# Performance work log

Measured on AMD Instinct MI355X. Metric: run time of the kernel, lower is better.

Reference implementation:

```python
import jax, jax.numpy as jnp
import numpy as np

B, T, H, PRED = 16384, 8, 256, 12


def _cell(x, h, c, Wih, Whh, bih, bhh):
    # PyTorch LSTM gate order: i, f, g, o
    g = x @ Wih.T + h @ Whh.T + bih + bhh
    i, f, gg, o = jnp.split(g, 4, axis=-1)
    c = jax.nn.sigmoid(f) * c + jax.nn.sigmoid(i) * jnp.tanh(gg)
    h = jax.nn.sigmoid(o) * jnp.tanh(c)
    return h, c


def _run_seq(x, layers):
    # stacked LSTM over full sequence, zero initial state; x: [B, T, D]
    b = x.shape[0]
    inp = x
    hs, cs = [], []
    for (Wih, Whh, bih, bhh) in layers:
        h0 = jnp.zeros((b, Whh.shape[1]), x.dtype)

        def step(carry, xt, Wih=Wih, Whh=Whh, bih=bih, bhh=bhh):
            h, c = _cell(xt, carry[0], carry[1], Wih, Whh, bih, bhh)
            return (h, c), h

        (h, c), out = jax.lax.scan(step, (h0, h0), jnp.swapaxes(inp, 0, 1))
        inp = jnp.swapaxes(out, 0, 1)
        hs.append(h)
        cs.append(c)
    return inp, jnp.stack(hs), jnp.stack(cs)


def _step_stack(x, hs, cs, layers):
    # single-timestep pass through stacked LSTM; hs/cs: [L, B, H]
    inp = x
    nh, nc = [], []
    for l, (Wih, Whh, bih, bhh) in enumerate(layers):
        h, c = _cell(inp, hs[l], cs[l], Wih, Whh, bih, bhh)
        inp = h
        nh.append(h)
        nc.append(c)
    return inp, jnp.stack(nh), jnp.stack(nc)


def _forward(x, l1_Wih0, l1_Whh0, l1_bih0, l1_bhh0, l1_Wih1, l1_Whh1, l1_bih1, l1_bhh1,
             l2_Wih0, l2_Whh0, l2_bih0, l2_bhh0, l2_Wih1, l2_Whh1, l2_bih1, l2_bhh1,
             fc1_w, fc1_b, fc2_w, fc2_b):
    L1 = [(l1_Wih0, l1_Whh0, l1_bih0, l1_bhh0), (l1_Wih1, l1_Whh1, l1_bih1, l1_bhh1)]
    L2 = [(l2_Wih0, l2_Whh0, l2_bih0, l2_bhh0), (l2_Wih1, l2_Whh1, l2_bih1, l2_bhh1)]
    out1, h1, c1 = _run_seq(x, L1)           # encode observed track
    _, h2, c2 = _run_seq(out1, L2)
    pos = x[:, -1, :]

    def dec(carry, _):
        pos, h1, c1, h2, c2 = carry
        o1, h1, c1 = _step_stack(pos, h1, c1, L1)
        o2, h2, c2 = _step_stack(o1, h2, c2, L2)
        delta = jax.nn.relu(o2 @ fc1_w.T + fc1_b) @ fc2_w.T + fc2_b
        pos = pos + delta
        return (pos, h1, c1, h2, c2), pos

    _, preds = jax.lax.scan(dec, (pos, h1, c1, h2, c2), None, length=PRED)
    return jnp.swapaxes(preds, 0, 1)  # [B, PRED, 2]


def setup_inputs() -> dict:
    key = jax.random.key(0)
    ks = iter(jax.random.split(key, 32))
    s = 1.0 / np.sqrt(H)  # matches PyTorch LSTM/Linear init scale

    def mk(shape):
        return jax.random.uniform(next(ks), shape, jnp.float32, -s, s)

    d = {"x": jax.random.normal(next(ks), (B, T, 2), jnp.float32)}
    for name, in_dim in [("l1", 2), ("l2", H)]:
        for layer in range(2):
            di = in_dim if layer == 0 else H
            d[f"{name}_Wih{layer}"] = mk((4 * H, di))
            d[f"{name}_Whh{layer}"] = mk((4 * H, H))
            d[f"{name}_bih{layer}"] = mk((4 * H,))
            d[f"{name}_bhh{layer}"] = mk((4 * H,))
    d["fc1_w"] = mk((H, H))
    d["fc1_b"] = mk((H,))
    d["fc2_w"] = mk((2, H))
    d["fc2_b"] = mk((2,))
    return d


def reference(x, l1_Wih0, l1_Whh0, l1_bih0, l1_bhh0, l1_Wih1, l1_Whh1, l1_bih1, l1_bhh1,
              l2_Wih0, l2_Whh0, l2_bih0, l2_bhh0, l2_Wih1, l2_Whh1, l2_bih1, l2_bhh1,
              fc1_w, fc1_b, fc2_w, fc2_b):
    return _forward(x, l1_Wih0, l1_Whh0, l1_bih0, l1_bhh0, l1_Wih1, l1_Whh1, l1_bih1, l1_bhh1,
                    l2_Wih0, l2_Whh0, l2_bih0, l2_bhh0, l2_Wih1, l2_Whh1, l2_bih1, l2_bhh1,
                    fc1_w, fc1_b, fc2_w, fc2_b)
```

## Files before the change

### kernel.cpp

```cpp
#include <hip/hip_runtime.h>
#include <stdint.h>

#define Bsz   16384
#define Tseq  8
#define NPRED 12

typedef __attribute__((ext_vector_type(4))) float    f32x4;
typedef _Float16 h16;
typedef __attribute__((ext_vector_type(8))) _Float16 h16x8;

__device__ __forceinline__ float sigf(float x)   { return 1.f / (1.f + __expf(-x)); }
__device__ __forceinline__ float tanh_f(float x) { return 1.f - 2.f / (__expf(2.f * x) + 1.f); }

__device__ __forceinline__ void gload_lds16(const void* g, void* l) {
  __builtin_amdgcn_global_load_lds(
      (const __attribute__((address_space(1))) void*)g,
      (__attribute__((address_space(3))) void*)l, 16, 0, 0);
}

__global__ void mark_r11(float* __restrict__ out) {
  if (blockIdx.x == 0 && threadIdx.x < 64) out[threadIdx.x] = 1000.0f;
}
__global__ void seed_r11(float* __restrict__ pos, const float* __restrict__ x) {
  int b = blockIdx.x * 256 + threadIdx.x;
  pos[2 * b]     = x[(size_t)b * 16 + 14];
  pos[2 * b + 1] = x[(size_t)b * 16 + 15];
}

__global__ void pack_w(h16* __restrict__ dst, const float* __restrict__ W0,
                       const float* __restrict__ W1, int ksplit, int Kw, int Np,
                       int gatePack) {
  int idx = blockIdx.x * 256 + threadIdx.x;
  if (idx >= Np * Kw) return;
  int np = idx / Kw, k = idx - np * Kw;
  int n = np;
  if (gatePack) {
    int jb = np >> 7, wc = (np >> 6) & 1, gi = (np >> 4) & 3, jr = np & 15;
    n = gi * 256 + jb * 32 + wc * 16 + jr;
  }
  float w = (k < ksplit) ? W0[(size_t)n * ksplit + k]
                         : W1[(size_t)n * (Kw - ksplit) + (k - ksplit)];
  int KB = Kw >> 6;
  int jb = np >> 7, r = np & 127, kb = k >> 6;
  uint32_t byte = (uint32_t)(jb * KB + kb) * 16384u + (uint32_t)r * 128u
                + ((2u * (uint32_t)(k & 63)) ^ (uint32_t)((r & 7) << 4));
  *(h16*)((char*)dst + byte) = (h16)w;
}

__global__ void add_bias(float* __restrict__ dst, const float* __restrict__ a,
                         const float* __restrict__ b) {
  int i = blockIdx.x * 256 + threadIdx.x;
  if (i < 1024) dst[i] = a[i] + b[i];
}

__global__ void l0t0_pw(const float* __restrict__ x, const float* __restrict__ wih0,
                        const float* __restrict__ bias, float* __restrict__ Cst,
                        char* __restrict__ hout) {
  int gid = blockIdx.x * 256 + threadIdx.x;
  int b = gid >> 5, jb = (gid & 31) << 3;
  float x0 = x[(size_t)b * 16], x1 = x[(size_t)b * 16 + 1];
  float c[8]; h16 hh[8];
#pragma unroll
  for (int q = 0; q < 8; ++q) {
    int j = jb + q;
    float vi = bias[j]       + x0 * wih0[2 * j]           + x1 * wih0[2 * j + 1];
    float vg = bias[512 + j] + x0 * wih0[2 * (512 + j)]   + x1 * wih0[2 * (512 + j) + 1];
    float vo = bias[768 + j] + x0 * wih0[2 * (768 + j)]   + x1 * wih0[2 * (768 + j) + 1];
    float cn = sigf(vi) * tanh_f(vg);
    hh[q] = (h16)(sigf(vo) * tanh_f(cn));
    c[q] = cn;
  }
  *(f32x4*)(Cst + (size_t)b * 256 + jb)     = *(f32x4*)c;
  *(f32x4*)(Cst + (size_t)b * 256 + jb + 4) = *(f32x4*)(c + 4);
  *(h16x8*)(hout + (size_t)b * 512 + (((unsigned)jb * 2) ^ (unsigned)((b & 7) << 4))) = *(h16x8*)hh;
}

__device__ __forceinline__ void gemm_core(
    const char* A0, const char* A1, const char* Wp, int KB, int by, int m0,
    char* ldsA, char* ldsB, int tid, f32x4 acc[4][4]) {
  const int wave = tid >> 6, lane = tid & 63;
  const int rowa = tid >> 3;
  const int chb  = (tid & 7) * 16;

#pragma unroll
  for (int m = 0; m < 4; m++)
#pragma unroll
    for (int n = 0; n < 4; n++)
#pragma unroll
      for (int e = 0; e < 4; e++) acc[m][n][e] = 0.f;

  const char* aCur   = A0 + (size_t)(m0 + rowa) * 512 + chb;
  const char* a1Base = A1 + (size_t)(m0 + rowa) * 512 + chb;
  const char* wCur   = Wp + (size_t)by * KB * 16384 + rowa * 128 + chb;

  const int wr = wave >> 1, wc = wave & 1;

  for (int kb = 0; kb < KB; ++kb) {
    if (kb == 4) aCur = a1Base;
#pragma unroll
    for (int it = 0; it < 4; ++it) {
      gload_lds16(aCur + it * 16384, ldsA + it * 4096 + wave * 1024);
      gload_lds16(wCur + it * 4096,  ldsB + it * 4096 + wave * 1024);
    }
    __syncthreads();
#pragma unroll
    for (int kk = 0; kk < 2; ++kk) {
      const int kbyte = kk * 64 + (lane >> 4) * 16;
      h16x8 af[4], bfr[4];
#pragma unroll
      for (int mt = 0; mt < 4; ++mt) {
        int r = wr * 64 + mt * 16 + (lane & 15);
        af[mt] = *(const h16x8*)(ldsA + r * 128 + (kbyte ^ ((r & 7) << 4)));
      }
#pragma unroll
      for (int nt = 0; nt < 4; ++nt) {
        int c = wc * 64 + nt * 16 + (lane & 15);
        bfr[nt] = *(const h16x8*)(ldsB + c * 128 + (kbyte ^ ((c & 7) << 4)));
      }
#pragma unroll
      for (int mt = 0; mt < 4; ++mt)
#pragma unroll
        for (int nt = 0; nt < 4; ++nt)
          acc[mt][nt] = __builtin_amdgcn_mfma_f32_16x16x32_f16(af[mt], bfr[nt], acc[mt][nt], 0, 0, 0);
    }
    __syncthreads();
    aCur += 128;
    wCur += 16384;
  }
}

__device__ __forceinline__ void lstm_epilogue(
    f32x4 acc[4][4], int m0, int n0, int tid, const float* bias,
    const float* wih0, const float* xbase, int xstride, int hasx, int skipc,
    float* Cst, char* hout) {
  const int wave = tid >> 6, lane = tid & 63;
  const int wr = wave >> 1, wc = wave & 1;
  const int j = (n0 >> 2) + wc * 16 + (lane & 15);
  const float bi = bias[j], bff = bias[256 + j], bg = bias[512 + j], bo = bias[768 + j];
  float wi0 = 0, wi1 = 0, wf0 = 0, wf1 = 0, wg0 = 0, wg1 = 0, wo0 = 0, wo1 = 0;
  if (hasx) {
    wi0 = wih0[2 * j];           wi1 = wih0[2 * j + 1];
    wf0 = wih0[2 * (256 + j)];   wf1 = wih0[2 * (256 + j) + 1];
    wg0 = wih0[2 * (512 + j)];   wg1 = wih0[2 * (512 + j) + 1];
    wo0 = wih0[2 * (768 + j)];   wo1 = wih0[2 * (768 + j) + 1];
  }
#pragma unroll
  for (int mt = 0; mt < 4; ++mt) {
#pragma unroll
    for (int e = 0; e < 4; e++) {
      const int b = m0 + wr * 64 + mt * 16 + (lane >> 4) * 4 + e;
      float vi = acc[mt][0][e] + bi;
      float vf = acc[mt][1][e] + bff;
      float vg = acc[mt][2][e] + bg;
      float vo = acc[mt][3][e] + bo;
      if (hasx) {
        const float x0 = xbase[(size_t)b * xstride];
        const float x1 = xbase[(size_t)b * xstride + 1];
        vi += x0 * wi0 + x1 * wi1;
        vf += x0 * wf0 + x1 * wf1;
        vg += x0 * wg0 + x1 * wg1;
        vo += x0 * wo0 + x1 * wo1;
      }
      const size_t ci = (size_t)b * 256 + j;
      float cn = sigf(vi) * tanh_f(vg);
      if (!skipc) cn += sigf(vf) * Cst[ci];
      float h = sigf(vo) * tanh_f(cn);
      Cst[ci] = cn;
      *(h16*)(hout + (size_t)b * 512 + (((unsigned)j * 2) ^ (unsigned)((b & 7) << 4))) = (h16)h;
    }
  }
}

struct CellDesc {
  const char* A0; const char* A1; const char* Wp;
  const float* bias; const float* wih0; const float* xbase;
  float* Cst; char* hout;
  int Kw; int xstride; int hasx; int skipc;
};
struct Fused4 { CellDesc c[4]; };

__global__ __launch_bounds__(256, 4) void cells_diag(Fused4 args) {
  const int cellid = blockIdx.x >> 10;
  const int lid    = blockIdx.x & 1023;
  const CellDesc d = args.c[cellid];

  __shared__ __align__(16) char lds[32768];
  const int tid = threadIdx.x;

  int swz = (lid & 7) * 128 + (lid >> 3);
  const int by = swz & 7, bx = swz >> 3;
  const int m0 = bx * 128, n0 = by * 128;

  f32x4 acc[4][4];
  gemm_core(d.A0, d.A1, d.Wp, d.Kw >> 6, by, m0, lds, lds + 16384, tid, acc);
  lstm_epilogue(acc, m0, n0, tid, d.bias, d.wih0, d.xbase, d.xstride, d.hasx,
                d.skipc, d.Cst, d.hout);
}

template <int NSEG, int HASX>
__global__ __launch_bounds__(256, 4) void cell_gemm(
    const char* __restrict__ A0, const char* __restrict__ A1,
    const char* __restrict__ Wp, int Kw,
    const float* __restrict__ bias, const float* __restrict__ wih0,
    const float* __restrict__ xbase, int xstride,
    float* __restrict__ Cst, char* __restrict__ hout) {
  __shared__ __align__(16) char lds[32768];
  const int tid = threadIdx.x;

  int lid = blockIdx.x;
  int chunkv = gridDim.x >> 3;
  int swz = (lid & 7) * chunkv + (lid >> 3);
  const int by = swz % 8, bx = swz / 8;
  const int m0 = bx * 128, n0 = by * 128;

  f32x4 acc[4][4];
  gemm_core(A0, NSEG == 2 ? A1 : A0, Wp, Kw >> 6, by, m0, lds, lds + 16384, tid, acc);
  lstm_epilogue(acc, m0, n0, tid, bias, wih0, xbase, xstride, HASX, 0, Cst, hout);
}

__global__ __launch_bounds__(256) void fc_head(
    const char* __restrict__ A, const char* __restrict__ Wp,
    const float* __restrict__ b1, const float* __restrict__ w2,
    const float* __restrict__ b2, float* __restrict__ pos,
    float* __restrict__ out, int s) {
  __shared__ __align__(16) char lds[34304];
  const int tid = threadIdx.x;
  const int m0 = blockIdx.x * 128;
  const int wave = tid >> 6, lane = tid & 63;
  const int wr = wave >> 1, wc = wave & 1;
  const int bl2 = tid >> 1, comp = tid & 1;

  float a = 0.f;
  for (int half = 0; half < 2; ++half) {
    f32x4 acc[4][4];
    gemm_core(A, A, Wp, 4, half, m0, lds, lds + 16384, tid, acc);
    h16* strip = (h16*)lds;
#pragma unroll
    for (int nt = 0; nt < 4; ++nt) {
      const int n = half * 128 + wc * 64 + nt * 16 + (lane & 15);
      const int nl = wc * 64 + nt * 16 + (lane & 15);
      const float bn = b1[n];
#pragma unroll
      for (int mt = 0; mt < 4; ++mt)
#pragma unroll
        for (int e = 0; e < 4; e++) {
          const int bl = wr * 64 + mt * 16 + (lane >> 4) * 4 + e;
          float v = acc[mt][nt][e] + bn;
          strip[bl * 134 + nl] = (h16)(v > 0.f ? v : 0.f);
        }
    }
    __syncthreads();
    const float* wrow = w2 + comp * 256 + half * 128;
#pragma unroll 8
    for (int n = 0; n < 128; ++n)
      a += (float)strip[bl2 * 134 + n] * wrow[n];
    __syncthreads();
  }
  const size_t b = (size_t)(m0 + bl2);
  float p = pos[2 * b + comp] + a + b2[comp];
  pos[2 * b + comp] = p;
  out[b * (NPRED * 2) + s * 2 + comp] = p;
}

extern "C" void kernel_launch(void* const* d_in, const int* in_sizes, int n_in,
                              void* d_out, int out_size, void* d_ws, size_t ws_size,
                              hipStream_t stream) {
  const float* x      = (const float*)d_in[0];
  const float* Wih[4] = {(const float*)d_in[1], (const float*)d_in[5],
                         (const float*)d_in[9], (const float*)d_in[13]};
  const float* Whh[4] = {(const float*)d_in[2], (const float*)d_in[6],
                         (const float*)d_in[10], (const float*)d_in[14]};
  const float* bih[4] = {(const float*)d_in[3], (const float*)d_in[7],
                         (const float*)d_in[11], (const float*)d_in[15]};
  const float* bhh[4] = {(const float*)d_in[4], (const float*)d_in[8],
                         (const float*)d_in[12], (const float*)d_in[16]};
  const float* fc1_w = (const float*)d_in[17];
  const float* fc1_b = (const float*)d_in[18];
  const float* fc2_w = (const float*)d_in[19];
  const float* fc2_b = (const float*)d_in[20];

  char* ws = (char*)d_ws;
  size_t off = 0;
  auto alloc = [&](size_t bytes) -> char* {
    char* p = ws + off;
    off += (bytes + 255) & ~(size_t)255;
    return p;
  };

  float* Cs[4];
  for (int l = 0; l < 4; l++) Cs[l] = (float*)alloc((size_t)Bsz * 256 * 4);
  char* h10[2] = {alloc((size_t)Bsz * 512), alloc((size_t)Bsz * 512)};
  char* sl[2]  = {alloc((size_t)Bsz * 512), alloc((size_t)Bsz * 512)};
  char* h20[2] = {alloc((size_t)Bsz * 512), alloc((size_t)Bsz * 512)};
  char* h21[2] = {alloc((size_t)Bsz * 512), alloc((size_t)Bsz * 512)};
  float* pos = (float*)alloc((size_t)Bsz * 2 * 4);
  float* biasc = (float*)alloc(4 * 1024 * 4);
  h16* wp10 = (h16*)alloc((size_t)1024 * 256 * 2);
  h16* wp[3];
  for (int i = 0; i < 3; i++) wp[i] = (h16*)alloc((size_t)1024 * 512 * 2);
  h16* wpf1 = (h16*)alloc((size_t)256 * 256 * 2);

  if (ws_size < off) {
    mark_r11<<<dim3(1), dim3(64), 0, stream>>>((float*)d_out);
    return;
  }

  seed_r11<<<dim3(Bsz / 256), dim3(256), 0, stream>>>(pos, x);

  pack_w<<<dim3((1024 * 256 + 255) / 256), dim3(256), 0, stream>>>(wp10, Whh[0], Whh[0], 256, 256, 1024, 1);
  pack_w<<<dim3((1024 * 512 + 255) / 256), dim3(256), 0, stream>>>(wp[0], Wih[1], Whh[1], 256, 512, 1024, 1);
  pack_w<<<dim3((1024 * 512 + 255) / 256), dim3(256), 0, stream>>>(wp[1], Wih[2], Whh[2], 256, 512, 1024, 1);
  pack_w<<<dim3((1024 * 512 + 255) / 256), dim3(256), 0, stream>>>(wp[2], Wih[3], Whh[3], 256, 512, 1024, 1);
  pack_w<<<dim3((256 * 256 + 255) / 256), dim3(256), 0, stream>>>(wpf1, fc1_w, fc1_w, 256, 256, 256, 0);
  for (int l = 0; l < 4; l++)
    add_bias<<<dim3(4), dim3(256), 0, stream>>>(biasc + l * 1024, bih[l], bhh[l]);

  char* hbuf[4][2] = {{h10[0], h10[1]}, {sl[0], sl[1]}, {h20[0], h20[1]}, {h21[0], h21[1]}};
  const h16* wpl[4] = {wp10, wp[0], wp[1], wp[2]};
  for (int d = 0; d <= 10; d++) {
    if (d == 0) {
      l0t0_pw<<<dim3(2048), dim3(256), 0, stream>>>(x, Wih[0], biasc, Cs[0], hbuf[0][0]);
      continue;
    }
    Fused4 args;
    int nc = 0;
    for (int l = 0; l < 4; l++) {
      int t = d - l;
      if (t < 0 || t >= Tseq) continue;
      CellDesc& cd = args.c[nc++];
      cd.A0 = (l == 0) ? hbuf[0][(t - 1) & 1] : hbuf[l - 1][t & 1];
      cd.A1 = (l > 0 && t > 0) ? hbuf[l][(t - 1) & 1] : cd.A0;
      cd.Wp = (const char*)wpl[l];
      cd.bias = biasc + l * 1024;
      cd.wih0 = (l == 0) ? Wih[0] : nullptr;
      cd.xbase = (l == 0) ? (x + t * 2) : nullptr;
      cd.Cst = Cs[l];
      cd.hout = hbuf[l][t & 1];
      cd.Kw = (l == 0 || t == 0) ? 256 : 512;
      cd.xstride = 16;
      cd.hasx = (l == 0) ? 1 : 0;
      cd.skipc = (t == 0) ? 1 : 0;
    }
    cells_diag<<<dim3(nc * 1024), dim3(256), 0, stream>>>(args);
  }

  for (int s = 0; s < NPRED; s++) {
    int u = Tseq + s, cur = u & 1, prev = cur ^ 1;
    cell_gemm<1, 1><<<dim3(1024), dim3(256), 0, stream>>>(
        h10[prev], h10[prev], (const char*)wp10, 256, biasc, Wih[0], pos, 2, Cs[0], h10[cur]);
    cell_gemm<2, 0><<<dim3(1024), dim3(256), 0, stream>>>(
        h10[cur], sl[prev], (const char*)wp[0], 512, biasc + 1024, nullptr, nullptr, 0, Cs[1], sl[cur]);
    cell_gemm<2, 0><<<dim3(1024), dim3(256), 0, stream>>>(
        sl[cur], h20[prev], (const char*)wp[1], 512, biasc + 2048, nullptr, nullptr, 0, Cs[2], h20[cur]);
    cell_gemm<2, 0><<<dim3(1024), dim3(256), 0, stream>>>(
        h20[cur], h21[prev], (const char*)wp[2], 512, biasc + 3072, nullptr, nullptr, 0, Cs[3], h21[cur]);
    fc_head<<<dim3(128), dim3(256), 0, stream>>>(
        h21[cur], (const char*)wpf1, fc1_b, fc2_w, fc2_b, pos, (float*)d_out, s);
  }
}
```

Baseline: 2.353 ms.

## Fuse decoder loop into cooperative persistent kernel and store cell state in fp16

Replaces the 60 per-step decoder kernel launches with one cooperative kernel that loops over prediction steps and separates each layer cell and the FC head with grid-wide syncs. This removes launch overhead and inter-kernel gaps. It also halves cell-state memory traffic by storing the LSTM c state in fp16 instead of fp32, which lowers the precision of the recurrent state. The grid syncs add their own cost, and the head phase runs on only 128 of the 1024 blocks while the others wait.

```diff
diff --git a/kernel.cpp b/kernel.cpp
--- a/kernel.cpp
+++ b/kernel.cpp
@@ -1,5 +1,8 @@
 #include <hip/hip_runtime.h>
+#include <hip/hip_cooperative_groups.h>
 #include <stdint.h>
+
+namespace cg = cooperative_groups;
 
 #define Bsz   16384
 #define Tseq  8
@@ -18,10 +21,10 @@
       (__attribute__((address_space(3))) void*)l, 16, 0, 0);
 }
 
-__global__ void mark_r11(float* __restrict__ out) {
+__global__ void mark_r12(float* __restrict__ out) {
   if (blockIdx.x == 0 && threadIdx.x < 64) out[threadIdx.x] = 1000.0f;
 }
-__global__ void seed_r11(float* __restrict__ pos, const float* __restrict__ x) {
+__global__ void seed_r12(float* __restrict__ pos, const float* __restrict__ x) {
   int b = blockIdx.x * 256 + threadIdx.x;
   pos[2 * b]     = x[(size_t)b * 16 + 14];
   pos[2 * b + 1] = x[(size_t)b * 16 + 15];
@@ -54,12 +57,12 @@
 }
 
 __global__ void l0t0_pw(const float* __restrict__ x, const float* __restrict__ wih0,
-                        const float* __restrict__ bias, float* __restrict__ Cst,
+                        const float* __restrict__ bias, h16* __restrict__ Cst,
                         char* __restrict__ hout) {
   int gid = blockIdx.x * 256 + threadIdx.x;
   int b = gid >> 5, jb = (gid & 31) << 3;
   float x0 = x[(size_t)b * 16], x1 = x[(size_t)b * 16 + 1];
-  float c[8]; h16 hh[8];
+  h16 cc[8]; h16 hh[8];
 #pragma unroll
   for (int q = 0; q < 8; ++q) {
     int j = jb + q;
@@ -68,10 +71,9 @@
     float vo = bias[768 + j] + x0 * wih0[2 * (768 + j)]   + x1 * wih0[2 * (768 + j) + 1];
     float cn = sigf(vi) * tanh_f(vg);
     hh[q] = (h16)(sigf(vo) * tanh_f(cn));
-    c[q] = cn;
-  }
-  *(f32x4*)(Cst + (size_t)b * 256 + jb)     = *(f32x4*)c;
-  *(f32x4*)(Cst + (size_t)b * 256 + jb + 4) = *(f32x4*)(c + 4);
+    cc[q] = (h16)cn;
+  }
+  *(h16x8*)(Cst + (size_t)b * 256 + jb) = *(h16x8*)cc;
   *(h16x8*)(hout + (size_t)b * 512 + (((unsigned)jb * 2) ^ (unsigned)((b & 7) << 4))) = *(h16x8*)hh;
 }
 
@@ -132,7 +134,7 @@
 __device__ __forceinline__ void lstm_epilogue(
     f32x4 acc[4][4], int m0, int n0, int tid, const float* bias,
     const float* wih0, const float* xbase, int xstride, int hasx, int skipc,
-    float* Cst, char* hout) {
+    h16* Cst, char* hout) {
   const int wave = tid >> 6, lane = tid & 63;
   const int wr = wave >> 1, wc = wave & 1;
   const int j = (n0 >> 2) + wc * 16 + (lane & 15);
@@ -163,18 +165,58 @@
       }
       const size_t ci = (size_t)b * 256 + j;
       float cn = sigf(vi) * tanh_f(vg);
-      if (!skipc) cn += sigf(vf) * Cst[ci];
+      if (!skipc) cn += sigf(vf) * (float)Cst[ci];
       float h = sigf(vo) * tanh_f(cn);
-      Cst[ci] = cn;
+      Cst[ci] = (h16)cn;
       *(h16*)(hout + (size_t)b * 512 + (((unsigned)j * 2) ^ (unsigned)((b & 7) << 4))) = (h16)h;
     }
   }
+}
+
+__device__ __forceinline__ void head_body(
+    const char* A, const char* Wp, const float* b1, const float* w2,
+    const float* b2, float* pos, float* out, int s, int blk, int tid, char* lds) {
+  const int m0 = blk * 128;
+  const int wave = tid >> 6, lane = tid & 63;
+  const int wr = wave >> 1, wc = wave & 1;
+  const int bl2 = tid >> 1, comp = tid & 1;
+
+  float a = 0.f;
+  for (int half = 0; half < 2; ++half) {
+    f32x4 acc[4][4];
+    gemm_core(A, A, Wp, 4, half, m0, lds, lds + 16384, tid, acc);
+    h16* strip = (h16*)lds;
+#pragma unroll
+    for (int nt = 0; nt < 4; ++nt) {
+      const int n = half * 128 + wc * 64 + nt * 16 + (lane & 15);
+      const int nl = wc * 64 + nt * 16 + (lane & 15);
+      const float bn = b1[n];
+#pragma unroll
+      for (int mt = 0; mt < 4; ++mt)
+#pragma unroll
+        for (int e = 0; e < 4; e++) {
+          const int bl = wr * 64 + mt * 16 + (lane >> 4) * 4 + e;
+          float v = acc[mt][nt][e] + bn;
+          strip[bl * 134 + nl] = (h16)(v > 0.f ? v : 0.f);
+        }
+    }
+    __syncthreads();
+    const float* wrow = w2 + comp * 256 + half * 128;
+#pragma unroll 8
+    for (int n = 0; n < 128; ++n)
+      a += (float)strip[bl2 * 134 + n] * wrow[n];
+    __syncthreads();
+  }
+  const size_t b = (size_t)(m0 + bl2);
+  float p = pos[2 * b + comp] + a + b2[comp];
+  pos[2 * b + comp] = p;
+  out[b * (NPRED * 2) + s * 2 + comp] = p;
 }
 
 struct CellDesc {
   const char* A0; const char* A1; const char* Wp;
   const float* bias; const float* wih0; const float* xbase;
-  float* Cst; char* hout;
+  h16* Cst; char* hout;
   int Kw; int xstride; int hasx; int skipc;
 };
 struct Fused4 { CellDesc c[4]; };
@@ -195,6 +237,56 @@
   gemm_core(d.A0, d.A1, d.Wp, d.Kw >> 6, by, m0, lds, lds + 16384, tid, acc);
   lstm_epilogue(acc, m0, n0, tid, d.bias, d.wih0, d.xbase, d.xstride, d.hasx,
                 d.skipc, d.Cst, d.hout);
+}
+
+struct DecArgs {
+  char* hb0[2]; char* hb1[2]; char* hb2[2]; char* hb3[2];
+  h16* Cs0; h16* Cs1; h16* Cs2; h16* Cs3;
+  const char* wp10; const char* wp0; const char* wp1; const char* wp2; const char* wpf1;
+  const float* biasc; const float* wih0;
+  const float* fc1_b; const float* fc2_w; const float* fc2_b;
+  float* pos; float* out;
+};
+
+__global__ __launch_bounds__(256, 4) void decoder_coop(DecArgs a) {
+  cg::grid_group grid = cg::this_grid();
+  __shared__ __align__(16) char lds[34304];
+  const int tid = threadIdx.x;
+  const int lid = blockIdx.x;
+  int swz = (lid & 7) * 128 + (lid >> 3);
+  const int by = swz & 7, bx = swz >> 3;
+  const int m0 = bx * 128, n0 = by * 128;
+
+  for (int s = 0; s < NPRED; ++s) {
+    const int u = Tseq + s, cur = u & 1, prev = cur ^ 1;
+    {
+      f32x4 acc[4][4];
+      gemm_core(a.hb0[prev], a.hb0[prev], a.wp10, 4, by, m0, lds, lds + 16384, tid, acc);
+      lstm_epilogue(acc, m0, n0, tid, a.biasc, a.wih0, a.pos, 2, 1, 0, a.Cs0, a.hb0[cur]);
+    }
+    __threadfence();  grid.sync();
+    {
+      f32x4 acc[4][4];
+      gemm_core(a.hb0[cur], a.hb1[prev], a.wp0, 8, by, m0, lds, lds + 16384, tid, acc);
+      lstm_epilogue(acc, m0, n0, tid, a.biasc + 1024, nullptr, nullptr, 0, 0, 0, a.Cs1, a.hb1[cur]);
+    }
+    __threadfence();  grid.sync();
+    {
+      f32x4 acc[4][4];
+      gemm_core(a.hb1[cur], a.hb2[prev], a.wp1, 8, by, m0, lds, lds + 16384, tid, acc);
+      lstm_epilogue(acc, m0, n0, tid, a.biasc + 2048, nullptr, nullptr, 0, 0, 0, a.Cs2, a.hb2[cur]);
+    }
+    __threadfence();  grid.sync();
+    {
+      f32x4 acc[4][4];
+      gemm_core(a.hb2[cur], a.hb3[prev], a.wp2, 8, by, m0, lds, lds + 16384, tid, acc);
+      lstm_epilogue(acc, m0, n0, tid, a.biasc + 3072, nullptr, nullptr, 0, 0, 0, a.Cs3, a.hb3[cur]);
+    }
+    __threadfence();  grid.sync();
+    if (lid < 128)
+      head_body(a.hb3[cur], a.wpf1, a.fc1_b, a.fc2_w, a.fc2_b, a.pos, a.out, s, lid, tid, lds);
+    __threadfence();  grid.sync();
+  }
 }
 
 template <int NSEG, int HASX>
@@ -203,16 +295,14 @@
     const char* __restrict__ Wp, int Kw,
     const float* __restrict__ bias, const float* __restrict__ wih0,
     const float* __restrict__ xbase, int xstride,
-    float* __restrict__ Cst, char* __restrict__ hout) {
+    h16* __restrict__ Cst, char* __restrict__ hout) {
   __shared__ __align__(16) char lds[32768];
   const int tid = threadIdx.x;
-
   int lid = blockIdx.x;
   int chunkv = gridDim.x >> 3;
   int swz = (lid & 7) * chunkv + (lid >> 3);
   const int by = swz % 8, bx = swz / 8;
   const int m0 = bx * 128, n0 = by * 128;
-
   f32x4 acc[4][4];
   gemm_core(A0, NSEG == 2 ? A1 : A0, Wp, Kw >> 6, by, m0, lds, lds + 16384, tid, acc);
   lstm_epilogue(acc, m0, n0, tid, bias, wih0, xbase, xstride, HASX, 0, Cst, hout);
@@ -224,42 +314,7 @@
     const float* __restrict__ b2, float* __restrict__ pos,
     float* __restrict__ out, int s) {
   __shared__ __align__(16) char lds[34304];
-  const int tid = threadIdx.x;
-  const int m0 = blockIdx.x * 128;
-  const int wave = tid >> 6, lane = tid & 63;
-  const int wr = wave >> 1, wc = wave & 1;
-  const int bl2 = tid >> 1, comp = tid & 1;
-
-  float a = 0.f;
-  for (int half = 0; half < 2; ++half) {
-    f32x4 acc[4][4];
-    gemm_core(A, A, Wp, 4, half, m0, lds, lds + 16384, tid, acc);
-    h16* strip = (h16*)lds;
-#pragma unroll
-    for (int nt = 0; nt < 4; ++nt) {
-      const int n = half * 128 + wc * 64 + nt * 16 + (lane & 15);
-      const int nl = wc * 64 + nt * 16 + (lane & 15);
-      const float bn = b1[n];
-#pragma unroll
-      for (int mt = 0; mt < 4; ++mt)
-#pragma unroll
-        for (int e = 0; e < 4; e++) {
-          const int bl = wr * 64 + mt * 16 + (lane >> 4) * 4 + e;
-          float v = acc[mt][nt][e] + bn;
-          strip[bl * 134 + nl] = (h16)(v > 0.f ? v : 0.f);
-        }
-    }
-    __syncthreads();
-    const float* wrow = w2 + comp * 256 + half * 128;
-#pragma unroll 8
-    for (int n = 0; n < 128; ++n)
-      a += (float)strip[bl2 * 134 + n] * wrow[n];
-    __syncthreads();
-  }
-  const size_t b = (size_t)(m0 + bl2);
-  float p = pos[2 * b + comp] + a + b2[comp];
-  pos[2 * b + comp] = p;
-  out[b * (NPRED * 2) + s * 2 + comp] = p;
+  head_body(A, Wp, b1, w2, b2, pos, out, s, blockIdx.x, threadIdx.x, lds);
 }
 
 extern "C" void kernel_launch(void* const* d_in, const int* in_sizes, int n_in,
@@ -287,8 +342,8 @@
     return p;
   };
 
-  float* Cs[4];
-  for (int l = 0; l < 4; l++) Cs[l] = (float*)alloc((size_t)Bsz * 256 * 4);
+  h16* Cs[4];
+  for (int l = 0; l < 4; l++) Cs[l] = (h16*)alloc((size_t)Bsz * 256 * 2);
   char* h10[2] = {alloc((size_t)Bsz * 512), alloc((size_t)Bsz * 512)};
   char* sl[2]  = {alloc((size_t)Bsz * 512), alloc((size_t)Bsz * 512)};
   char* h20[2] = {alloc((size_t)Bsz * 512), alloc((size_t)Bsz * 512)};
@@ -301,11 +356,11 @@
   h16* wpf1 = (h16*)alloc((size_t)256 * 256 * 2);
 
   if (ws_size < off) {
-    mark_r11<<<dim3(1), dim3(64), 0, stream>>>((float*)d_out);
+    mark_r12<<<dim3(1), dim3(64), 0, stream>>>((float*)d_out);
     return;
   }
 
-  seed_r11<<<dim3(Bsz / 256), dim3(256), 0, stream>>>(pos, x);
+  seed_r12<<<dim3(Bsz / 256), dim3(256), 0, stream>>>(pos, x);
 
   pack_w<<<dim3((1024 * 256 + 255) / 256), dim3(256), 0, stream>>>(wp10, Whh[0], Whh[0], 256, 256, 1024, 1);
   pack_w<<<dim3((1024 * 512 + 255) / 256), dim3(256), 0, stream>>>(wp[0], Wih[1], Whh[1], 256, 512, 1024, 1);
@@ -344,6 +399,29 @@
     cells_diag<<<dim3(nc * 1024), dim3(256), 0, stream>>>(args);
   }
 
+  int maxb = 0;
+  hipError_t oe = hipOccupancyMaxActiveBlocksPerMultiprocessor(&maxb, decoder_coop, 256, 0);
+  bool useCoop = (oe == hipSuccess && maxb >= 4);
+
+  if (useCoop) {
+    DecArgs da;
+    da.hb0[0] = h10[0]; da.hb0[1] = h10[1];
+    da.hb1[0] = sl[0];  da.hb1[1] = sl[1];
+    da.hb2[0] = h20[0]; da.hb2[1] = h20[1];
+    da.hb3[0] = h21[0]; da.hb3[1] = h21[1];
+    da.Cs0 = Cs[0]; da.Cs1 = Cs[1]; da.Cs2 = Cs[2]; da.Cs3 = Cs[3];
+    da.wp10 = (const char*)wp10; da.wp0 = (const char*)wp[0];
+    da.wp1 = (const char*)wp[1]; da.wp2 = (const char*)wp[2];
+    da.wpf1 = (const char*)wpf1;
+    da.biasc = biasc; da.wih0 = Wih[0];
+    da.fc1_b = fc1_b; da.fc2_w = fc2_w; da.fc2_b = fc2_b;
+    da.pos = pos; da.out = (float*)d_out;
+    void* kargs[] = { &da };
+    hipError_t le = hipLaunchCooperativeKernel(decoder_coop, dim3(1024), dim3(256),
+                                               kargs, 0, stream);
+    if (le == hipSuccess) return;
+  }
+
   for (int s = 0; s < NPRED; s++) {
     int u = Tseq + s, cur = u & 1, prev = cur ^ 1;
     cell_gemm<1, 1><<<dim3(1024), dim3(256), 0, stream>>>(
```

New measurement: 2.317 ms. Within noise of the previous version (-1.5%).
